# Kernel optimization log

Hardware: AMD Instinct MI355X
Metric: run time of the kernel (lower is better)

The kernel has to match this reference:

```python
import jax, jax.numpy as jnp
import numpy as np

B = 512; S = 6; Q = 2            # meta-batch, n_way*k_shot, n_way*q_query
DIM = 64; IMG = 28; N_WAY = 2
HEADS = 4; HD = DIM // HEADS     # retrieval heads / head dim
EPS = 1e-5


def _pool_mat(inp, out):
    # exact torch AdaptiveAvgPool2d windowing as a matrix [out, inp]
    P = np.zeros((out, inp), np.float32)
    for i in range(out):
        s = (i * inp) // out
        e = -((-(i + 1) * inp) // out)
        P[i, s:e] = 1.0 / (e - s)
    return jnp.asarray(P)

P28 = _pool_mat(IMG, 8)  # 28 -> 8; subsequent 8 -> 8 pools are identity


def _gelu(x):
    return jax.nn.gelu(x, approximate=False)


def _conv(x, w, b):
    y = jax.lax.conv_general_dilated(x, w, (1, 1), ((1, 1), (1, 1)),
                                     dimension_numbers=('NCHW', 'OIHW', 'NCHW'))
    return y + b[None, :, None, None]


def _bn(x, p):
    # p rows: gamma, beta, running_mean, running_var (eval-mode BatchNorm2d)
    g, bt, m, v = p[0], p[1], p[2], p[3]
    sc = g / jnp.sqrt(v + EPS)
    return (x - m[None, :, None, None]) * sc[None, :, None, None] + bt[None, :, None, None]


def _img_in(x, c1w, c1b, bn1, c2w, c2b, bn2, c3w, c3b, bn3, c4w, c4b, bn4, lin_w):
    h = _bn(_conv(x, c1w, c1b), bn1)
    h = jnp.einsum('oi,ncij,pj->ncop', P28, h, P28)   # adaptive avg pool 28x28 -> 8x8
    h = _gelu(h)                                       # dropout is identity in eval
    h = _gelu(_bn(_conv(h, c2w, c2b), bn2))
    h = _gelu(_bn(_conv(h, c3w, c3b), bn3))
    h = _gelu(_bn(_conv(h, c4w, c4b), bn4))            # -> [N,1,8,8]
    h = h.reshape(h.shape[0], -1)                      # [N,64]
    return h @ lin_w.T                                 # Linear(64 -> DIM, no bias)


def _net(x, w1, w2):
    # x: [B,K,D]; w1,w2: [B,D,D] batched fast weights
    h = jnp.einsum('bed,bkd->bke', w1, x)
    ah = _gelu(h)
    y = jnp.einsum('bed,bkd->bke', w2, ah)
    return y, h


def _get_lor(x, w1, w2, r_q, r_k, r_v, r_o, ln_w, ln_b):
    b, k, _ = x.shape
    q, _ = _net(x, w1, w2)
    qh = jnp.einsum('nhd,bkd->bknh', r_q, q)
    sc = jnp.einsum('bknh,rnh->bknr', qh, r_k) / (HD ** 0.5)
    p = jax.nn.softmax(sc, axis=-1)
    lor = jnp.einsum('bknr,rnh->bknh', p, r_v).reshape(b, k, DIM)
    lor = jnp.einsum('de,bkd->bke', r_o, lor)
    z = lor + x
    mu = z.mean(-1, keepdims=True)
    var = ((z - mu) ** 2).mean(-1, keepdims=True)
    return (z - mu) / jnp.sqrt(var + EPS) * ln_w + ln_b


def _forward(query_w, sxs, qxs, inner_lr, c1w, c1b, bn1, c2w, c2b, bn2, c3w, c3b, bn3,
             c4w, c4b, bn4, lin_w, emb, w1, w2, tags, r_q, r_k, r_v, r_o, ln_w, ln_b,
             sys, qys):
    b = query_w.shape[0]
    s = sxs.shape[1]
    q = qxs.shape[1]
    feats = lambda im: _img_in(im.reshape(-1, 1, IMG, IMG), c1w, c1b, bn1, c2w, c2b,
                               bn2, c3w, c3b, bn3, c4w, c4b, bn4, lin_w)
    sx = feats(sxs).reshape(b, s, DIM)
    qx = feats(qxs).reshape(b, q, DIM)
    qe = tags[4]
    w1b = jnp.broadcast_to(w1, (b, DIM, DIM))
    w2b = jnp.broadcast_to(w2, (b, DIM, DIM))
    bound = sx + emb[sys]                                          # [B,S,D]
    # all 4 tag variants for all S shots in one vectorized get_lor call
    inp = (bound[:, :, None, :] + tags[:4][None, None]).reshape(b, s * 4, DIM)
    lors = _get_lor(inp, w1b, w2b, r_q, r_k, r_v, r_o, ln_w, ln_b).reshape(b, s, 4, DIM)
    l1s, r1s, l2s, r2s = lors[:, :, 0], lors[:, :, 1], lors[:, :, 2], lors[:, :, 3]
    qw1 = w1[None] + jnp.einsum('bsl,bsr->blr', l1s, r1s)
    qw2 = w2[None] + jnp.einsum('bsl,bsr->blr', l2s, r2s)
    preds, _ = _net(qx + qe, qw1, qw2)                             # [B,Q,D]
    logits = jnp.einsum('ld,bqd->bql', emb, preds).reshape(-1, N_WAY)
    labels = qys.reshape(-1)
    ls = jax.nn.log_softmax(logits)
    task_loss = -jnp.take_along_axis(ls, labels[:, None], axis=1).mean()
    n_correct = (jnp.argmax(logits, axis=1) == labels).sum()
    return task_loss, n_correct, b * q


def setup_inputs() -> dict:
    key = jax.random.key(0)
    ks = jax.random.split(key, 24)
    rn = lambda i, sh, sc=1.0: sc * jax.random.normal(ks[i], sh, jnp.float32)
    def bnp(i, c):
        k0, k1, k2 = jax.random.split(ks[i], 3)
        return jnp.stack([1.0 + 0.1 * jax.random.normal(k0, (c,)),
                          0.1 * jax.random.normal(k1, (c,)),
                          0.1 * jax.random.normal(k2, (c,)),
                          0.5 + jax.random.uniform(jax.random.fold_in(ks[i], 3), (c,))])
    return {
        'query_w': rn(0, (B, DIM)),
        'sxs': rn(1, (B, S, IMG * IMG)),
        'qxs': rn(2, (B, Q, IMG * IMG)),
        'inner_lr': jnp.float32(0.1),
        'c1w': rn(3, (32, 1, 3, 3), 0.3), 'c1b': rn(4, (32,), 0.1), 'bn1': bnp(5, 32),
        'c2w': rn(6, (32, 32, 3, 3), 0.06), 'c2b': rn(7, (32,), 0.1), 'bn2': bnp(8, 32),
        'c3w': rn(9, (32, 32, 3, 3), 0.06), 'c3b': rn(10, (32,), 0.1), 'bn3': bnp(11, 32),
        'c4w': rn(12, (1, 32, 3, 3), 0.06), 'c4b': rn(13, (1,), 0.1), 'bn4': bnp(14, 1),
        'lin_w': rn(15, (DIM, 64), 0.125),
        'emb': rn(16, (N_WAY, DIM), 0.125),
        'w1': rn(17, (DIM, DIM), 0.125),
        'w2': rn(18, (DIM, DIM), 0.125),
        'tags': rn(19, (8, DIM), 0.125),
        'r_q': rn(20, (HEADS, HD, DIM), 0.125),
        'r_k': rn(21, (16, HEADS, HD), 0.25),
        'r_v': rn(22, (16, HEADS, HD), 0.25),
        'r_o': rn(23, (DIM, DIM), 0.125),
        'ln_w': 0.001 * jnp.ones((DIM,), jnp.float32),
        'ln_b': jnp.zeros((DIM,), jnp.float32),
        'sys': jax.random.randint(jax.random.fold_in(key, 100), (B, S), 0, N_WAY),
        'qys': jax.random.randint(jax.random.fold_in(key, 101), (B, Q), 0, N_WAY),
    }


def reference(query_w, sxs, qxs, inner_lr, c1w, c1b, bn1, c2w, c2b, bn2, c3w, c3b, bn3,
              c4w, c4b, bn4, lin_w, emb, w1, w2, tags, r_q, r_k, r_v, r_o, ln_w, ln_b,
              sys, qys):
    task_loss, n_correct, n_q = _forward(query_w, sxs, qxs, inner_lr, c1w, c1b, bn1,
                                         c2w, c2b, bn2, c3w, c3b, bn3, c4w, c4b, bn4,
                                         lin_w, emb, w1, w2, tags, r_q, r_k, r_v, r_o,
                                         ln_w, ln_b, sys, qys)
    return (task_loss, task_loss, jnp.float32(0.0), n_correct, n_q)
```

## Files before the change

kernel.cpp:

```cpp
#include <hip/hip_runtime.h>
#include <math.h>

constexpr int NSUP = 3072;
constexpr float EPSF = 1e-5f;

constexpr int WS_W1B  = 0;
constexpr int WS_B1   = 1024;
constexpr int WS_W2B  = 1056;
constexpr int WS_W3B  = 5664;
constexpr int WS_W4B  = 10272;
constexpr int WS_B4   = 10416;
constexpr int WS_B2   = 10420;
constexpr int WS_B3   = 10452;
constexpr int WS_HW1  = 10484;
constexpr int WS_HW2  = 12788;
constexpr int WS_HRQ  = 15092;
constexpr int WS_HROT = 17396;
constexpr int WS_RKB  = 19700;
constexpr int WS_RVT  = 20212;
constexpr int WS_PART = 20724;
constexpr int WS_FEATS= 21748;

using short8 = __attribute__((ext_vector_type(8))) short;
using f32x4  = __attribute__((ext_vector_type(4))) float;

__device__ __forceinline__ float gelu_f(float x) {
    float z  = fabsf(x) * 0.70710678118654752440f;
    float t  = __builtin_amdgcn_rcpf(__builtin_fmaf(0.3275911f, z, 1.0f));
    float p  = t * __builtin_fmaf(t,
                 __builtin_fmaf(t,
                   __builtin_fmaf(t,
                     __builtin_fmaf(t, 1.061405429f, -1.453152027f),
                     1.421413741f),
                   -0.284496736f),
                 0.254829592f);
    float e  = __expf(-z * z);
    float er = __builtin_fmaf(-p, e, 1.0f);
    float s  = copysignf(er, x);
    return 0.5f * x * (1.0f + s);
}
__device__ __forceinline__ unsigned short f2bf(float f) {
    unsigned u = __float_as_uint(f);
    return (unsigned short)((u + 0x7FFFu + ((u >> 16) & 1u)) >> 16);
}
__device__ __forceinline__ float bflo(unsigned u) { return __uint_as_float(u << 16); }
__device__ __forceinline__ float bfhi(unsigned u) { return __uint_as_float(u & 0xffff0000u); }

__global__ void __launch_bounds__(256) precompute_kernel(
    const float* __restrict__ c1w, const float* __restrict__ c1b, const float* __restrict__ bn1,
    const float* __restrict__ c2w, const float* __restrict__ c2b, const float* __restrict__ bn2,
    const float* __restrict__ c3w, const float* __restrict__ c3b, const float* __restrict__ bn3,
    const float* __restrict__ c4w, const float* __restrict__ c4b, const float* __restrict__ bn4,
    const float* __restrict__ w1, const float* __restrict__ w2,
    const float* __restrict__ rq, const float* __restrict__ ro,
    const float* __restrict__ rk, const float* __restrict__ rv,
    float* __restrict__ ws)
{
    const int gid = blockIdx.x * 256 + threadIdx.x;
    const int gsz = gridDim.x * 256;

    unsigned short* w1b = (unsigned short*)(ws + WS_W1B);
    for (int v = gid; v < 2048; v += gsz) {
        int c8 = v & 7, colx = (v >> 3) & 15, qd = (v >> 7) & 3, hh = (v >> 9) & 1, kt = v >> 10;
        int tap = kt * 32 + qd * 8 + c8;
        int oc = hh * 16 + colx;
        unsigned short o = 0;
        if (tap < 36) {
            int tt = tap / 6, s = tap - tt * 6;
            float sum = 0.f;
            for (int di = 0; di < 3; ++di) {
                int a = tt - di; if (a < 0 || a > 3) continue;
                for (int dj = 0; dj < 3; ++dj) {
                    int bb = s - dj; if (bb < 0 || bb > 3) continue;
                    sum += c1w[oc * 9 + di * 3 + dj];
                }
            }
            float sc1 = bn1[oc] * rsqrtf(bn1[96 + oc] + EPSF);
            o = f2bf(sum * sc1 * (1.0f / 16.0f));
        }
        w1b[v] = o;
    }
    for (int c = gid; c < 32; c += gsz) {
        float sc1 = bn1[c] * rsqrtf(bn1[96 + c] + EPSF);
        ws[WS_B1 + c] = (c1b[c] - bn1[64 + c]) * sc1 + bn1[32 + c];
        float sc2 = bn2[c] * rsqrtf(bn2[96 + c] + EPSF);
        ws[WS_B2 + c] = (c2b[c] - bn2[64 + c]) * sc2 + bn2[32 + c];
        float sc3 = bn3[c] * rsqrtf(bn3[96 + c] + EPSF);
        ws[WS_B3 + c] = (c3b[c] - bn3[64 + c]) * sc3 + bn3[32 + c];
    }
    unsigned short* w2b = (unsigned short*)(ws + WS_W2B);
    unsigned short* w3b = (unsigned short*)(ws + WS_W3B);
    for (int v = gid; v < 9216; v += gsz) {
        int c8 = v & 7, colx = (v >> 3) & 15, qd = (v >> 7) & 3, hh = (v >> 9) & 1, tap = v >> 10;
        int oc = hh * 16 + colx;
        int ic = qd * 8 + c8;
        float sc2 = bn2[oc] * rsqrtf(bn2[96 + oc] + EPSF);
        float sc3 = bn3[oc] * rsqrtf(bn3[96 + oc] + EPSF);
        w2b[v] = f2bf(c2w[oc * 288 + ic * 9 + tap] * sc2);
        w3b[v] = f2bf(c3w[oc * 288 + ic * 9 + tap] * sc3);
    }
    {
        unsigned short* w4b = (unsigned short*)(ws + WS_W4B);
        float sc4 = bn4[0] * rsqrtf(bn4[3] + EPSF);
        for (int v = gid; v < 288; v += gsz) {
            int tap = v >> 5, ic = v & 31;
            w4b[v] = f2bf(c4w[ic * 9 + tap] * sc4);
        }
        if (gid == 0) ws[WS_B4] = (c4b[0] - bn4[2]) * sc4 + bn4[1];
    }
    unsigned short* hw1 = (unsigned short*)(ws + WS_HW1);
    unsigned short* hw2 = (unsigned short*)(ws + WS_HW2);
    unsigned short* hrq = (unsigned short*)(ws + WS_HRQ);
    unsigned short* hro = (unsigned short*)(ws + WS_HROT);
    for (int v = gid; v < 4608; v += gsz) {
        int e = v / 72, d = v - e * 72;
        unsigned short a = 0, b = 0, c = 0, r = 0;
        if (d < 64) {
            a = f2bf(w1[e * 64 + d]);
            b = f2bf(w2[e * 64 + d]);
            c = f2bf(rq[e * 64 + d]);
            r = f2bf(ro[d * 64 + e]);
        }
        hw1[v] = a; hw2[v] = b; hrq[v] = c; hro[v] = r;
    }
    unsigned short* rkb = (unsigned short*)(ws + WS_RKB);
    unsigned short* rvt = (unsigned short*)(ws + WS_RVT);
    for (int v = gid; v < 1024; v += gsz) {
        int nn = v >> 8, x = (v >> 4) & 15, y = v & 15;
        rkb[v] = f2bf(rk[x * 64 + nn * 16 + y] * 0.25f);
        rvt[v] = f2bf(rv[y * 64 + nn * 16 + x]);
    }
}

__device__ __forceinline__ void conv32g(const unsigned short* __restrict__ A,
                                        const unsigned short* __restrict__ Wg,
                                        int col, int quad, f32x4 (&acc)[4][2])
{
    int ab[4];
    #pragma unroll
    for (int mt = 0; mt < 4; ++mt) {
        int px = mt * 16 + col;
        ab[mt] = quad * 800 + ((px >> 3) * 10 + (px & 7)) * 8;
        acc[mt][0] = (f32x4){0,0,0,0};
        acc[mt][1] = (f32x4){0,0,0,0};
    }
    #pragma unroll
    for (int dr = 0; dr < 3; ++dr)
        #pragma unroll
        for (int dc = 0; dc < 3; ++dc) {
            int tap = dr * 3 + dc;
            short8 b0 = *(const short8*)(Wg + (((tap * 2 + 0) * 4 + quad) * 16 + col) * 8);
            short8 b1 = *(const short8*)(Wg + (((tap * 2 + 1) * 4 + quad) * 16 + col) * 8);
            #pragma unroll
            for (int mt = 0; mt < 4; ++mt) {
                short8 a = *(const short8*)(A + ab[mt] + (dr * 10 + dc) * 8);
                acc[mt][0] = __builtin_amdgcn_mfma_f32_16x16x32_bf16(a, b0, acc[mt][0], 0, 0, 0);
                acc[mt][1] = __builtin_amdgcn_mfma_f32_16x16x32_bf16(a, b1, acc[mt][1], 0, 0, 0);
            }
        }
}

__device__ __forceinline__ void conv_store4(unsigned short* __restrict__ A,
                                            const f32x4 (&acc)[4][2],
                                            float bi0, float bi1, int col, int quad)
{
    #pragma unroll
    for (int mt = 0; mt < 4; ++mt)
        #pragma unroll
        for (int reg = 0; reg < 4; ++reg) {
            int px = mt * 16 + quad * 4 + reg;
            int P = ((px >> 3) + 1) * 10 + (px & 7) + 1;
            A[(col >> 3) * 800 + P * 8 + (col & 7)]       = f2bf(gelu_f(acc[mt][0][reg] + bi0));
            A[(2 + (col >> 3)) * 800 + P * 8 + (col & 7)] = f2bf(gelu_f(acc[mt][1][reg] + bi1));
        }
}

__global__ void __launch_bounds__(256, 4) feats_kernel(
    const float* __restrict__ sxs, const float* __restrict__ qxs,
    const float* __restrict__ lin_w, const float* __restrict__ ws,
    float* __restrict__ feats)
{
    __shared__ __align__(16) unsigned short sAct[4][3200];
    __shared__ __align__(16) float sh4[4][64];

    const int t    = threadIdx.x;
    const int wv   = t >> 6;
    const int lane = t & 63;
    const int col  = lane & 15;
    const int quad = lane >> 4;
    const int n    = blockIdx.x * 4 + wv;

    unsigned short* A = sAct[wv];

    float bi1a = ws[WS_B1 + col], bi1b = ws[WS_B1 + 16 + col];
    float bi2a = ws[WS_B2 + col], bi2b = ws[WS_B2 + 16 + col];
    float bi3a = ws[WS_B3 + col], bi3b = ws[WS_B3 + 16 + col];
    float b4   = ws[WS_B4];

    {
        const float* img = (n < NSUP) ? (sxs + (size_t)n * 784) : (qxs + (size_t)(n - NSUP) * 784);
        const float4* sv = (const float4*)img;
        #pragma unroll
        for (int j = 0; j < 4; ++j) {
            int idx = j * 64 + lane;
            if (idx < 196) {
                float4 v = sv[idx];
                ushort4 o = { f2bf(v.x), f2bf(v.y), f2bf(v.z), f2bf(v.w) };
                *(ushort4*)(A + idx * 4) = o;
            }
        }
    }

    f32x4 acc[4][2];
    {
        const unsigned short* w1g = (const unsigned short*)(ws + WS_W1B);
        short8 b00 = *(const short8*)(w1g + ((0 * 4 + quad) * 16 + col) * 8);
        short8 b01 = *(const short8*)(w1g + ((1 * 4 + quad) * 16 + col) * 8);
        short8 b10 = *(const short8*)(w1g + ((2 * 4 + quad) * 16 + col) * 8);
        short8 b11 = *(const short8*)(w1g + ((3 * 4 + quad) * 16 + col) * 8);
        int ttj[8], ssj[8];
        #pragma unroll
        for (int j = 0; j < 8; ++j) {
            int k = quad * 8 + j;
            ttj[j] = k / 6; ssj[j] = k - ttj[j] * 6;
        }
        #pragma unroll
        for (int mt = 0; mt < 4; ++mt) {
            acc[mt][0] = (f32x4){0,0,0,0};
            acc[mt][1] = (f32x4){0,0,0,0};
            int px = mt * 16 + col;
            int sr = (((px >> 3) * 7) >> 1) - 1;
            int sc = (((px & 7) * 7) >> 1) - 1;
            short8 a0;
            #pragma unroll
            for (int j = 0; j < 8; ++j) {
                int rr = sr + ttj[j], cc = sc + ssj[j];
                bool ok = ((unsigned)rr < 28u) && ((unsigned)cc < 28u);
                int off = ok ? (rr * 28 + cc) : 0;
                unsigned short hv = A[off];
                a0[j] = ok ? (short)hv : (short)0;
            }
            acc[mt][0] = __builtin_amdgcn_mfma_f32_16x16x32_bf16(a0, b00, acc[mt][0], 0, 0, 0);
            acc[mt][1] = __builtin_amdgcn_mfma_f32_16x16x32_bf16(a0, b01, acc[mt][1], 0, 0, 0);
            short8 a1 = {0,0,0,0,0,0,0,0};
            if (quad == 0) {
                #pragma unroll
                for (int j = 0; j < 4; ++j) {
                    int rr = sr + 5, cc = sc + 2 + j;
                    bool ok = ((unsigned)rr < 28u) && ((unsigned)cc < 28u);
                    int off = ok ? (rr * 28 + cc) : 0;
                    unsigned short hv = A[off];
                    a1[j] = ok ? (short)hv : (short)0;
                }
            }
            acc[mt][0] = __builtin_amdgcn_mfma_f32_16x16x32_bf16(a1, b10, acc[mt][0], 0, 0, 0);
            acc[mt][1] = __builtin_amdgcn_mfma_f32_16x16x32_bf16(a1, b11, acc[mt][1], 0, 0, 0);
        }
    }
    {
        uint4 z4 = {0, 0, 0, 0};
        #pragma unroll
        for (int it = 0; it < 3; ++it) {
            int h = lane + it * 64;
            if (h < 144) {
                int pi = h >> 2, ch = h & 3;
                int P;
                if (pi < 10)      P = pi;
                else if (pi < 20) P = 90 + (pi - 10);
                else { int k = pi - 20; int r = 1 + (k >> 1); P = r * 10 + (k & 1) * 9; }
                ((uint4*)A)[ch * 100 + P] = z4;
            }
        }
    }
    conv_store4(A, acc, bi1a, bi1b, col, quad);

    conv32g(A, (const unsigned short*)(ws + WS_W2B), col, quad, acc);
    conv_store4(A, acc, bi2a, bi2b, col, quad);
    conv32g(A, (const unsigned short*)(ws + WS_W3B), col, quad, acc);
    conv_store4(A, acc, bi3a, bi3b, col, quad);

    {
        f32x4 acc4[4];
        int ab[4];
        #pragma unroll
        for (int mt = 0; mt < 4; ++mt) {
            int px = mt * 16 + col;
            ab[mt] = quad * 800 + ((px >> 3) * 10 + (px & 7)) * 8;
            acc4[mt] = (f32x4){0,0,0,0};
        }
        const unsigned short* w4g = (const unsigned short*)(ws + WS_W4B);
        #pragma unroll
        for (int dr = 0; dr < 3; ++dr)
            #pragma unroll
            for (int dc = 0; dc < 3; ++dc) {
                int tap = dr * 3 + dc;
                short8 b = *(const short8*)(w4g + tap * 32 + quad * 8);
                #pragma unroll
                for (int mt = 0; mt < 4; ++mt) {
                    short8 a = *(const short8*)(A + ab[mt] + (dr * 10 + dc) * 8);
                    acc4[mt] = __builtin_amdgcn_mfma_f32_16x16x32_bf16(a, b, acc4[mt], 0, 0, 0);
                }
            }
        if (col < 4) {
            f32x4 v = acc4[0];
            if (col == 1) v = acc4[1];
            else if (col == 2) v = acc4[2];
            else if (col == 3) v = acc4[3];
            #pragma unroll
            for (int reg = 0; reg < 4; ++reg)
                sh4[wv][col * 16 + quad * 4 + reg] = gelu_f(v[reg] + b4);
        }
    }

    {
        const float4* lw = (const float4*)(lin_w + (size_t)lane * 64);
        const float4* hp = (const float4*)sh4[wv];
        float acc2 = 0.f;
        #pragma unroll
        for (int j = 0; j < 16; ++j) {
            float4 w = lw[j], h = hp[j];
            acc2 += w.x * h.x + w.y * h.y + w.z * h.z + w.w * h.w;
        }
        feats[n * 64 + lane] = acc2;
    }
}

__device__ __forceinline__ void head_gemm(const unsigned short* __restrict__ Ab,
                                          const unsigned short* __restrict__ Bw,
                                          int col, int quad, int wvid, f32x4 res[2])
{
    #pragma unroll
    for (int u = 0; u < 2; ++u) {
        int tau = wvid + u * 4;
        int mt = tau & 1, nt = tau >> 1;
        f32x4 acc = {0, 0, 0, 0};
        #pragma unroll
        for (int kt = 0; kt < 2; ++kt) {
            short8 a = *(const short8*)(Ab + (mt * 16 + col) * 72 + kt * 32 + quad * 8);
            short8 b = *(const short8*)(Bw + (nt * 16 + col) * 72 + kt * 32 + quad * 8);
            acc = __builtin_amdgcn_mfma_f32_16x16x32_bf16(a, b, acc, 0, 0, 0);
        }
        res[u] = acc;
    }
}

__global__ void __launch_bounds__(256, 2) head_kernel(
    const float* __restrict__ emb, const float* __restrict__ tags,
    const float* __restrict__ lnw, const float* __restrict__ lnb,
    const int* __restrict__ sys, const int* __restrict__ qys,
    const float* __restrict__ ws, const float* __restrict__ feats,
    float* __restrict__ part)
{
    __shared__ __align__(16) unsigned short sW1B[4608], sW2B[4608], sRQB[4608], sROT[4608];
    __shared__ __align__(16) unsigned short bufA[2304], bufB[2304];
    __shared__ __align__(16) unsigned short sP[2048];
    __shared__ __align__(16) float sXf[1536];
    __shared__ __align__(16) float s_xq[128], s_ah[128], s_yp[128];
    __shared__ float s_t1[12], s_t2[12], s_mu[24], s_rs[24], s_lg[4];

    const int t    = threadIdx.x;
    const int b    = blockIdx.x;
    const int wvid = t >> 6;
    const int col  = t & 15;
    const int quad = (t >> 4) & 3;

    for (int i = t; i < 576; i += 256) {
        ((uint4*)sW1B)[i] = ((const uint4*)(ws + WS_HW1))[i];
        ((uint4*)sW2B)[i] = ((const uint4*)(ws + WS_HW2))[i];
        ((uint4*)sRQB)[i] = ((const uint4*)(ws + WS_HRQ))[i];
        ((uint4*)sROT)[i] = ((const uint4*)(ws + WS_HROT))[i];
    }
    {
        uint4 z = {0, 0, 0, 0};
        if (t < 72) {
            ((uint4*)(bufA + 1728))[t] = z;
            ((uint4*)(bufB + 1728))[t] = z;
        }
        if (t < 64)
            ((uint4*)(sP + 1536))[t] = z;
    }
    for (int idx = t; idx < 1536; idx += 256) {
        int k = idx >> 6, e = idx & 63;
        int s = k >> 2, tg = k & 3;
        int cls = sys[b * 6 + s];
        float v = feats[(b * 6 + s) * 64 + e] + emb[cls * 64 + e] + tags[tg * 64 + e];
        sXf[idx] = v;
        bufA[k * 72 + e] = f2bf(v);
    }
    __syncthreads();

    f32x4 r[2];
    head_gemm(bufA, sW1B, col, quad, wvid, r);
    #pragma unroll
    for (int u = 0; u < 2; ++u) {
        int tau = wvid + u * 4, mt = tau & 1, nt = tau >> 1;
        #pragma unroll
        for (int reg = 0; reg < 4; ++reg) {
            int row = mt * 16 + quad * 4 + reg;
            if (row < 24) bufB[row * 72 + nt * 16 + col] = f2bf(gelu_f(r[u][reg]));
        }
    }
    __syncthreads();
    head_gemm(bufB, sW2B, col, quad, wvid, r);
    #pragma unroll
    for (int u = 0; u < 2; ++u) {
        int tau = wvid + u * 4, mt = tau & 1, nt = tau >> 1;
        #pragma unroll
        for (int reg = 0; reg < 4; ++reg) {
            int row = mt * 16 + quad * 4 + reg;
            if (row < 24) bufA[row * 72 + nt * 16 + col] = f2bf(r[u][reg]);
        }
    }
    __syncthreads();
    head_gemm(bufA, sRQB, col, quad, wvid, r);
    #pragma unroll
    for (int u = 0; u < 2; ++u) {
        int tau = wvid + u * 4, mt = tau & 1, nt = tau >> 1;
        #pragma unroll
        for (int reg = 0; reg < 4; ++reg) {
            int row = mt * 16 + quad * 4 + reg;
            if (row < 24) bufB[row * 72 + nt * 16 + col] = f2bf(r[u][reg]);
        }
    }
    __syncthreads();

    {
        const int nh = wvid;
        const unsigned short* rkB = (const unsigned short*)(ws + WS_RKB) + nh * 256;
        const unsigned short* rvT = (const unsigned short*)(ws + WS_RVT) + nh * 256;
        const short8 zz = {0,0,0,0,0,0,0,0};
        const bool lo = (quad < 2);
        short8 bK = lo ? *(const short8*)(rkB + col * 16 + quad * 8) : zz;
        short8 a0 = lo ? *(const short8*)(bufB + col * 72 + nh * 16 + quad * 8) : zz;
        short8 a1 = lo ? *(const short8*)(bufB + (16 + col) * 72 + nh * 16 + quad * 8) : zz;
        f32x4 s0 = __builtin_amdgcn_mfma_f32_16x16x32_bf16(a0, bK, (f32x4){0,0,0,0}, 0, 0, 0);
        f32x4 s1 = __builtin_amdgcn_mfma_f32_16x16x32_bf16(a1, bK, (f32x4){0,0,0,0}, 0, 0, 0);
        #pragma unroll
        for (int reg = 0; reg < 4; ++reg) {
            float v = s0[reg];
            float m = v;
            m = fmaxf(m, __shfl_xor(m, 1)); m = fmaxf(m, __shfl_xor(m, 2));
            m = fmaxf(m, __shfl_xor(m, 4)); m = fmaxf(m, __shfl_xor(m, 8));
            float p = __expf(v - m);
            float su = p;
            su += __shfl_xor(su, 1); su += __shfl_xor(su, 2);
            su += __shfl_xor(su, 4); su += __shfl_xor(su, 8);
            sP[(quad * 4 + reg) * 64 + nh * 16 + col] = f2bf(p / su);
            v = s1[reg];
            m = v;
            m = fmaxf(m, __shfl_xor(m, 1)); m = fmaxf(m, __shfl_xor(m, 2));
            m = fmaxf(m, __shfl_xor(m, 4)); m = fmaxf(m, __shfl_xor(m, 8));
            p = __expf(v - m);
            su = p;
            su += __shfl_xor(su, 1); su += __shfl_xor(su, 2);
            su += __shfl_xor(su, 4); su += __shfl_xor(su, 8);
            if (quad < 2) sP[(16 + quad * 4 + reg) * 64 + nh * 16 + col] = f2bf(p / su);
        }
        short8 bV  = lo ? *(const short8*)(rvT + col * 16 + quad * 8) : zz;
        short8 pa0 = lo ? *(const short8*)(sP + col * 64 + nh * 16 + quad * 8) : zz;
        short8 pa1 = lo ? *(const short8*)(sP + (16 + col) * 64 + nh * 16 + quad * 8) : zz;
        f32x4 o0 = __builtin_amdgcn_mfma_f32_16x16x32_bf16(pa0, bV, (f32x4){0,0,0,0}, 0, 0, 0);
        f32x4 o1 = __builtin_amdgcn_mfma_f32_16x16x32_bf16(pa1, bV, (f32x4){0,0,0,0}, 0, 0, 0);
        #pragma unroll
        for (int reg = 0; reg < 4; ++reg) {
            bufA[(quad * 4 + reg) * 72 + nh * 16 + col] = f2bf(o0[reg]);
            int tok = 16 + quad * 4 + reg;
            if (tok < 24) bufA[tok * 72 + nh * 16 + col] = f2bf(o1[reg]);
        }
    }
    __syncthreads();

    head_gemm(bufA, sROT, col, quad, wvid, r);
    #pragma unroll
    for (int u = 0; u < 2; ++u) {
        int tau = wvid + u * 4, mt = tau & 1, nt = tau >> 1;
        #pragma unroll
        for (int reg = 0; reg < 4; ++reg) {
            int row = mt * 16 + quad * 4 + reg;
            if (row < 24) {
                int idx = row * 64 + nt * 16 + col;
                sXf[idx] = sXf[idx] + r[u][reg];
            }
        }
    }
    __syncthreads();

    if (t < 192) {
        int k = t >> 3, j = t & 7;
        const float4* zp = (const float4*)(sXf + k * 64 + j * 8);
        float4 v0 = zp[0], v1 = zp[1];
        float sx_ = v0.x + v0.y + v0.z + v0.w + v1.x + v1.y + v1.z + v1.w;
        sx_ += __shfl_xor(sx_, 1); sx_ += __shfl_xor(sx_, 2); sx_ += __shfl_xor(sx_, 4);
        float mu = sx_ * (1.0f / 64.0f);
        float d0 = v0.x - mu, d1 = v0.y - mu, d2 = v0.z - mu, d3 = v0.w - mu;
        float d4 = v1.x - mu, d5 = v1.y - mu, d6 = v1.z - mu, d7 = v1.w - mu;
        float vv = d0*d0 + d1*d1 + d2*d2 + d3*d3 + d4*d4 + d5*d5 + d6*d6 + d7*d7;
        vv += __shfl_xor(vv, 1); vv += __shfl_xor(vv, 2); vv += __shfl_xor(vv, 4);
        if (j == 0) {
            s_mu[k] = mu;
            s_rs[k] = 1.0f / sqrtf(vv * (1.0f / 64.0f) + EPSF);
        }
    }
    __syncthreads();
    for (int idx = t; idx < 1536; idx += 256) {
        int k = idx >> 6, e = idx & 63;
        float v = (sXf[idx] - s_mu[k]) * s_rs[k] * lnw[e] + lnb[e];
        bufB[k * 72 + e] = f2bf(v);
    }
    if (t < 128) {
        int q = t >> 6, e = t & 63;
        s_xq[t] = feats[(NSUP + b * 2 + q) * 64 + e] + tags[256 + e];
    }
    __syncthreads();

    if (t < 96) {
        int idx = t >> 3, j = t & 7;
        int q = idx / 6, s = idx - q * 6;
        uint4 u = ((const uint4*)(bufB + (s * 4 + 1) * 72))[j];
        const float* x = s_xq + q * 64 + j * 8;
        float d = bflo(u.x)*x[0] + bfhi(u.x)*x[1] + bflo(u.y)*x[2] + bfhi(u.y)*x[3]
                + bflo(u.z)*x[4] + bfhi(u.z)*x[5] + bflo(u.w)*x[6] + bfhi(u.w)*x[7];
        d += __shfl_xor(d, 1); d += __shfl_xor(d, 2); d += __shfl_xor(d, 4);
        if (j == 0) s_t1[idx] = d;
    }
    __syncthreads();
    if (t < 128) {
        int q = t >> 6, e = t & 63;
        const uint4* wp = (const uint4*)(sW1B + e * 72);
        const float* xp = s_xq + q * 64;
        float acc = 0.f;
        #pragma unroll
        for (int j = 0; j < 8; ++j) {
            uint4 u = wp[j];
            const float* x = xp + j * 8;
            acc += bflo(u.x)*x[0] + bfhi(u.x)*x[1] + bflo(u.y)*x[2] + bfhi(u.y)*x[3]
                 + bflo(u.z)*x[4] + bfhi(u.z)*x[5] + bflo(u.w)*x[6] + bfhi(u.w)*x[7];
        }
        #pragma unroll
        for (int s = 0; s < 6; ++s)
            acc += bflo((unsigned)bufB[(s * 4 + 0) * 72 + e]) * s_t1[q * 6 + s];
        s_ah[t] = gelu_f(acc);
    }
    __syncthreads();
    if (t < 96) {
        int idx = t >> 3, j = t & 7;
        int q = idx / 6, s = idx - q * 6;
        uint4 u = ((const uint4*)(bufB + (s * 4 + 3) * 72))[j];
        const float* x = s_ah + q * 64 + j * 8;
        float d = bflo(u.x)*x[0] + bfhi(u.x)*x[1] + bflo(u.y)*x[2] + bfhi(u.y)*x[3]
                + bflo(u.z)*x[4] + bfhi(u.z)*x[5] + bflo(u.w)*x[6] + bfhi(u.w)*x[7];
        d += __shfl_xor(d, 1); d += __shfl_xor(d, 2); d += __shfl_xor(d, 4);
        if (j == 0) s_t2[idx] = d;
    }
    __syncthreads();
    if (t < 128) {
        int q = t >> 6, e = t & 63;
        const uint4* wp = (const uint4*)(sW2B + e * 72);
        const float* xp = s_ah + q * 64;
        float acc = 0.f;
        #pragma unroll
        for (int j = 0; j < 8; ++j) {
            uint4 u = wp[j];
            const float* x = xp + j * 8;
            acc += bflo(u.x)*x[0] + bfhi(u.x)*x[1] + bflo(u.y)*x[2] + bfhi(u.y)*x[3]
                 + bflo(u.z)*x[4] + bfhi(u.z)*x[5] + bflo(u.w)*x[6] + bfhi(u.w)*x[7];
        }
        #pragma unroll
        for (int s = 0; s < 6; ++s)
            acc += bflo((unsigned)bufB[(s * 4 + 2) * 72 + e]) * s_t2[q * 6 + s];
        s_yp[t] = acc;
    }
    __syncthreads();
    if (t < 32) {
        int q = t >> 4, ll = (t >> 3) & 1, j = t & 7;
        const float* ep = emb + ll * 64 + j * 8;
        const float* yp = s_yp + q * 64 + j * 8;
        float d = ep[0]*yp[0] + ep[1]*yp[1] + ep[2]*yp[2] + ep[3]*yp[3]
                + ep[4]*yp[4] + ep[5]*yp[5] + ep[6]*yp[6] + ep[7]*yp[7];
        d += __shfl_xor(d, 1); d += __shfl_xor(d, 2); d += __shfl_xor(d, 4);
        if (j == 0) s_lg[q * 2 + ll] = d;
    }
    __syncthreads();
    if (t == 0) {
        float lsum = 0.f, corr = 0.f;
        #pragma unroll
        for (int q = 0; q < 2; ++q) {
            float l0 = s_lg[q * 2], l1 = s_lg[q * 2 + 1];
            int lab = qys[b * 2 + q];
            float m = fmaxf(l0, l1);
            float lse = m + logf(expf(l0 - m) + expf(l1 - m));
            lsum += -((lab ? l1 : l0) - lse);
            int pred = (l1 > l0) ? 1 : 0;
            corr += (pred == lab) ? 1.0f : 0.0f;
        }
        part[b] = lsum;
        part[512 + b] = corr;
    }
}

__global__ void __launch_bounds__(256) finalize_kernel(const float* __restrict__ part,
                                                       float* __restrict__ out)
{
    __shared__ float sl[256], sc[256];
    const int t = threadIdx.x;
    sl[t] = part[t] + part[t + 256];
    sc[t] = part[512 + t] + part[768 + t];
    __syncthreads();
    for (int s = 128; s > 0; s >>= 1) {
        if (t < s) { sl[t] += sl[t + s]; sc[t] += sc[t + s]; }
        __syncthreads();
    }
    if (t == 0) {
        float loss = sl[0] * (1.0f / 1024.0f);
        out[0] = loss;
        out[1] = loss;
        out[2] = 0.0f;
        out[3] = sc[0];
        out[4] = 1024.0f;
    }
}

extern "C" void kernel_launch(void* const* d_in, const int* in_sizes, int n_in,
                              void* d_out, int out_size, void* d_ws, size_t ws_size,
                              hipStream_t stream)
{
    (void)in_sizes; (void)n_in; (void)out_size; (void)ws_size;
    const float* sxs  = (const float*)d_in[1];
    const float* qxs  = (const float*)d_in[2];
    const float* c1w  = (const float*)d_in[4];
    const float* c1b  = (const float*)d_in[5];
    const float* bn1  = (const float*)d_in[6];
    const float* c2w  = (const float*)d_in[7];
    const float* c2b  = (const float*)d_in[8];
    const float* bn2  = (const float*)d_in[9];
    const float* c3w  = (const float*)d_in[10];
    const float* c3b  = (const float*)d_in[11];
    const float* bn3  = (const float*)d_in[12];
    const float* c4w  = (const float*)d_in[13];
    const float* c4b  = (const float*)d_in[14];
    const float* bn4  = (const float*)d_in[15];
    const float* lin_w= (const float*)d_in[16];
    const float* emb  = (const float*)d_in[17];
    const float* w1   = (const float*)d_in[18];
    const float* w2   = (const float*)d_in[19];
    const float* tags = (const float*)d_in[20];
    const float* rq   = (const float*)d_in[21];
    const float* rk   = (const float*)d_in[22];
    const float* rv   = (const float*)d_in[23];
    const float* ro   = (const float*)d_in[24];
    const float* lnw  = (const float*)d_in[25];
    const float* lnb  = (const float*)d_in[26];
    const int*   sys  = (const int*)d_in[27];
    const int*   qys  = (const int*)d_in[28];

    float* ws  = (float*)d_ws;
    float* out = (float*)d_out;

    precompute_kernel<<<64, 256, 0, stream>>>(c1w, c1b, bn1, c2w, c2b, bn2,
                                              c3w, c3b, bn3, c4w, c4b, bn4,
                                              w1, w2, rq, ro, rk, rv, ws);
    feats_kernel<<<1024, 256, 0, stream>>>(sxs, qxs, lin_w, ws, ws + WS_FEATS);
    head_kernel<<<512, 256, 0, stream>>>(emb, tags, lnw, lnb, sys, qys,
                                         ws, ws + WS_FEATS, ws + WS_PART);
    finalize_kernel<<<1, 256, 0, stream>>>(ws + WS_PART, out);
}
```

Measured before the change: 167.8 us.

## Fuse finalize into head kernel via atomic counter, pad LDS channel stride

Removes the separate finalize kernel launch. The last head block to finish, detected with an atomic counter and threadfence, now performs the final loss and accuracy reduction using wave shuffles. The activation channel stride in LDS goes from 800 to 816 elements, likely to cut bank conflicts in the conv MFMA loads. LayerNorm is applied directly in registers with vectorized stores instead of a second pass through shared memory. This adds a grid-wide atomic and a memory-ordering dependency.

```diff
diff --git a/kernel.cpp b/kernel.cpp
--- a/kernel.cpp
+++ b/kernel.cpp
@@ -19,7 +19,11 @@
 constexpr int WS_RKB  = 19700;
 constexpr int WS_RVT  = 20212;
 constexpr int WS_PART = 20724;
-constexpr int WS_FEATS= 21748;
+constexpr int WS_CNT  = 21748;
+constexpr int WS_FEATS= 21752;
+
+constexpr int ACT_CS  = 816;
+constexpr int ACT_SZ  = 4 * ACT_CS;
 
 using short8 = __attribute__((ext_vector_type(8))) short;
 using f32x4  = __attribute__((ext_vector_type(4))) float;
@@ -58,6 +62,8 @@
 {
     const int gid = blockIdx.x * 256 + threadIdx.x;
     const int gsz = gridDim.x * 256;
+
+    if (gid == 0) *((unsigned*)(ws + WS_CNT)) = 0u;
 
     unsigned short* w1b = (unsigned short*)(ws + WS_W1B);
     for (int v = gid; v < 2048; v += gsz) {
@@ -140,7 +146,7 @@
     #pragma unroll
     for (int mt = 0; mt < 4; ++mt) {
         int px = mt * 16 + col;
-        ab[mt] = quad * 800 + ((px >> 3) * 10 + (px & 7)) * 8;
+        ab[mt] = quad * ACT_CS + ((px >> 3) * 10 + (px & 7)) * 8;
         acc[mt][0] = (f32x4){0,0,0,0};
         acc[mt][1] = (f32x4){0,0,0,0};
     }
@@ -170,8 +176,8 @@
         for (int reg = 0; reg < 4; ++reg) {
             int px = mt * 16 + quad * 4 + reg;
             int P = ((px >> 3) + 1) * 10 + (px & 7) + 1;
-            A[(col >> 3) * 800 + P * 8 + (col & 7)]       = f2bf(gelu_f(acc[mt][0][reg] + bi0));
-            A[(2 + (col >> 3)) * 800 + P * 8 + (col & 7)] = f2bf(gelu_f(acc[mt][1][reg] + bi1));
+            A[(col >> 3) * ACT_CS + P * 8 + (col & 7)]       = f2bf(gelu_f(acc[mt][0][reg] + bi0));
+            A[(2 + (col >> 3)) * ACT_CS + P * 8 + (col & 7)] = f2bf(gelu_f(acc[mt][1][reg] + bi1));
         }
 }
 
@@ -180,7 +186,7 @@
     const float* __restrict__ lin_w, const float* __restrict__ ws,
     float* __restrict__ feats)
 {
-    __shared__ __align__(16) unsigned short sAct[4][3200];
+    __shared__ __align__(16) unsigned short sAct[4][ACT_SZ];
     __shared__ __align__(16) float sh4[4][64];
 
     const int t    = threadIdx.x;
@@ -268,7 +274,7 @@
                 if (pi < 10)      P = pi;
                 else if (pi < 20) P = 90 + (pi - 10);
                 else { int k = pi - 20; int r = 1 + (k >> 1); P = r * 10 + (k & 1) * 9; }
-                ((uint4*)A)[ch * 100 + P] = z4;
+                ((uint4*)A)[ch * (ACT_CS / 8) + P] = z4;
             }
         }
     }
@@ -285,7 +291,7 @@
         #pragma unroll
         for (int mt = 0; mt < 4; ++mt) {
             int px = mt * 16 + col;
-            ab[mt] = quad * 800 + ((px >> 3) * 10 + (px & 7)) * 8;
+            ab[mt] = quad * ACT_CS + ((px >> 3) * 10 + (px & 7)) * 8;
             acc4[mt] = (f32x4){0,0,0,0};
         }
         const unsigned short* w4g = (const unsigned short*)(ws + WS_W4B);
@@ -348,19 +354,21 @@
     const float* __restrict__ emb, const float* __restrict__ tags,
     const float* __restrict__ lnw, const float* __restrict__ lnb,
     const int* __restrict__ sys, const int* __restrict__ qys,
-    const float* __restrict__ ws, const float* __restrict__ feats,
-    float* __restrict__ part)
+    float* __restrict__ ws, const float* __restrict__ feats,
+    float* __restrict__ out)
 {
     __shared__ __align__(16) unsigned short sW1B[4608], sW2B[4608], sRQB[4608], sROT[4608];
     __shared__ __align__(16) unsigned short bufA[2304], bufB[2304];
     __shared__ __align__(16) unsigned short sP[2048];
     __shared__ __align__(16) float sXf[1536];
     __shared__ __align__(16) float s_xq[128], s_ah[128], s_yp[128];
-    __shared__ float s_t1[12], s_t2[12], s_mu[24], s_rs[24], s_lg[4];
+    __shared__ float s_t1[12], s_t2[12], s_lg[4], s_red[8];
+    __shared__ int s_last;
 
     const int t    = threadIdx.x;
     const int b    = blockIdx.x;
     const int wvid = t >> 6;
+    const int lane = t & 63;
     const int col  = t & 15;
     const int quad = (t >> 4) & 3;
 
@@ -386,6 +394,10 @@
         float v = feats[(b * 6 + s) * 64 + e] + emb[cls * 64 + e] + tags[tg * 64 + e];
         sXf[idx] = v;
         bufA[k * 72 + e] = f2bf(v);
+    }
+    if (t < 128) {
+        int q = t >> 6, e = t & 63;
+        s_xq[t] = feats[(NSUP + b * 2 + q) * 64 + e] + tags[256 + e];
     }
     __syncthreads();
 
@@ -496,20 +508,16 @@
         float d4 = v1.x - mu, d5 = v1.y - mu, d6 = v1.z - mu, d7 = v1.w - mu;
         float vv = d0*d0 + d1*d1 + d2*d2 + d3*d3 + d4*d4 + d5*d5 + d6*d6 + d7*d7;
         vv += __shfl_xor(vv, 1); vv += __shfl_xor(vv, 2); vv += __shfl_xor(vv, 4);
-        if (j == 0) {
-            s_mu[k] = mu;
-            s_rs[k] = 1.0f / sqrtf(vv * (1.0f / 64.0f) + EPSF);
-        }
-    }
-    __syncthreads();
-    for (int idx = t; idx < 1536; idx += 256) {
-        int k = idx >> 6, e = idx & 63;
-        float v = (sXf[idx] - s_mu[k]) * s_rs[k] * lnw[e] + lnb[e];
-        bufB[k * 72 + e] = f2bf(v);
-    }
-    if (t < 128) {
-        int q = t >> 6, e = t & 63;
-        s_xq[t] = feats[(NSUP + b * 2 + q) * 64 + e] + tags[256 + e];
+        float rs = 1.0f / sqrtf(vv * (1.0f / 64.0f) + EPSF);
+        const float4* lwv = (const float4*)(lnw + j * 8);
+        const float4* lbv = (const float4*)(lnb + j * 8);
+        float4 w0 = lwv[0], w1_ = lwv[1], b0 = lbv[0], b1_ = lbv[1];
+        ushort4 o0 = { f2bf(d0 * rs * w0.x + b0.x), f2bf(d1 * rs * w0.y + b0.y),
+                       f2bf(d2 * rs * w0.z + b0.z), f2bf(d3 * rs * w0.w + b0.w) };
+        ushort4 o1 = { f2bf(d4 * rs * w1_.x + b1_.x), f2bf(d5 * rs * w1_.y + b1_.y),
+                       f2bf(d6 * rs * w1_.z + b1_.z), f2bf(d7 * rs * w1_.w + b1_.w) };
+        *(ushort4*)(bufB + k * 72 + j * 8)     = o0;
+        *(ushort4*)(bufB + k * 72 + j * 8 + 4) = o1;
     }
     __syncthreads();
 
@@ -581,6 +589,8 @@
         if (j == 0) s_lg[q * 2 + ll] = d;
     }
     __syncthreads();
+
+    float* part = ws + WS_PART;
     if (t == 0) {
         float lsum = 0.f, corr = 0.f;
         #pragma unroll
@@ -595,28 +605,34 @@
         }
         part[b] = lsum;
         part[512 + b] = corr;
-    }
-}
-
-__global__ void __launch_bounds__(256) finalize_kernel(const float* __restrict__ part,
-                                                       float* __restrict__ out)
-{
-    __shared__ float sl[256], sc[256];
-    const int t = threadIdx.x;
-    sl[t] = part[t] + part[t + 256];
-    sc[t] = part[512 + t] + part[768 + t];
-    __syncthreads();
-    for (int s = 128; s > 0; s >>= 1) {
-        if (t < s) { sl[t] += sl[t + s]; sc[t] += sc[t + s]; }
+        __threadfence();
+        unsigned old = atomicAdd((unsigned*)(ws + WS_CNT), 1u);
+        s_last = (old == 511) ? 1 : 0;
+    }
+    __syncthreads();
+
+    if (s_last) {
+        __threadfence();
+        float l = part[t] + part[t + 256];
+        float c = part[512 + t] + part[768 + t];
+        #pragma unroll
+        for (int off = 1; off < 64; off <<= 1) {
+            l += __shfl_xor(l, off);
+            c += __shfl_xor(c, off);
+        }
+        if (lane == 0) { s_red[wvid * 2] = l; s_red[wvid * 2 + 1] = c; }
         __syncthreads();
-    }
-    if (t == 0) {
-        float loss = sl[0] * (1.0f / 1024.0f);
-        out[0] = loss;
-        out[1] = loss;
-        out[2] = 0.0f;
-        out[3] = sc[0];
-        out[4] = 1024.0f;
+        if (t == 0) {
+            float L = 0.f, C = 0.f;
+            #pragma unroll
+            for (int w = 0; w < 4; ++w) { L += s_red[w * 2]; C += s_red[w * 2 + 1]; }
+            float loss = L * (1.0f / 1024.0f);
+            out[0] = loss;
+            out[1] = loss;
+            out[2] = 0.0f;
+            out[3] = C;
+            out[4] = 1024.0f;
+        }
     }
 }
 
@@ -661,6 +677,5 @@
                                               w1, w2, rq, ro, rk, rv, ws);
     feats_kernel<<<1024, 256, 0, stream>>>(sxs, qxs, lin_w, ws, ws + WS_FEATS);
     head_kernel<<<512, 256, 0, stream>>>(emb, tags, lnw, lnb, sys, qys,
-                                         ws, ws + WS_FEATS, ws + WS_PART);
-    finalize_kernel<<<1, 256, 0, stream>>>(ws + WS_PART, out);
-}
+                                         ws, ws + WS_FEATS, out);
+}
```

Measured after the change: 174.6 us. 1.04x slower.
